# Performance work log

Hardware: AMD Instinct MI355X
Metric: run time of the kernel (lower is better)

The kernel has to match this reference:

```python
import math
import jax, jax.numpy as jnp
import numpy as np

B, T, C, H = 2, 2048, 1024, 16
D = C // H


def get_slopes(n):
    def pow2_slopes(n):
        start = 2.0 ** (-(2.0 ** (-(math.log2(n) - 3))))
        return [start * (start ** i) for i in range(n)]
    if math.log2(n).is_integer():
        return pow2_slopes(n)
    c = 2 ** math.floor(math.log2(n))
    return pow2_slopes(c) + get_slopes(2 * c)[0::2][: n - c]


def setup_inputs() -> dict:
    key = jax.random.key(0)
    ks = jax.random.split(key, 5)
    std = 0.02
    x = jax.random.normal(ks[0], (B, T, C), dtype=jnp.float32)
    Wq = std * jax.random.normal(ks[1], (C, C), dtype=jnp.float32)
    Wk = std * jax.random.normal(ks[2], (C, C), dtype=jnp.float32)
    Wv = std * jax.random.normal(ks[3], (C, C), dtype=jnp.float32)
    Wo = (std / math.sqrt(24)) * jax.random.normal(ks[4], (C, C), dtype=jnp.float32)
    z = jnp.zeros((C,), dtype=jnp.float32)
    return {"x": x, "Wq": Wq, "bq": z, "Wk": Wk, "bk": z, "Wv": Wv, "bv": z, "Wo": Wo, "bo": z}


def reference(x, Wq, bq, Wk, bk, Wv, bv, Wo, bo):
    b, t, c = x.shape
    h, d = H, c // H
    # qkv projections: nn.Linear computes x @ W.T + b
    q = (x @ Wq.T + bq).reshape(b, t, h, d).transpose(0, 2, 1, 3)  # [B,H,T,D]
    k = (x @ Wk.T + bk).reshape(b, t, h, d).transpose(0, 2, 1, 3)
    v = (x @ Wv.T + bv).reshape(b, t, h, d).transpose(0, 2, 1, 3)

    att = jnp.einsum("bhqd,bhkd->bhqk", q, k) * (1.0 / math.sqrt(d))

    # ALiBi bias: -slope_h * (i - j) on the lower triangle, 0 above
    slopes = jnp.asarray(get_slopes(h), dtype=x.dtype)  # [H]
    i = jnp.arange(t)
    rel = jnp.tril(i[:, None] - i[None, :]).astype(x.dtype)  # [T,T]
    alibi = -slopes[:, None, None] * rel  # [H,T,T]
    att = att + alibi[None, :, :, :]

    causal = jnp.tril(jnp.ones((t, t), dtype=bool))
    att = jnp.where(causal[None, None, :, :], att, -jnp.inf)
    att = jax.nn.softmax(att, axis=-1)

    y = jnp.einsum("bhqk,bhkd->bhqd", att, v)
    y = y.transpose(0, 2, 1, 3).reshape(b, t, c)
    return y @ Wo.T + bo
```

## Files before the change

### kernel.cpp

```cpp
#include <hip/hip_runtime.h>
#include <hip/hip_bf16.h>
#include <cstdint>
#include <cstddef>

#define B_ 2
#define T_ 2048
#define C_ 1024
#define H_ 16
#define D_ 64
#define BT_ (B_*T_)
#define QKV_S 3072

typedef __bf16 bf16;
typedef __bf16 bf16x4 __attribute__((ext_vector_type(4)));
typedef __bf16 bf16x8 __attribute__((ext_vector_type(8)));
typedef float f32x4 __attribute__((ext_vector_type(4)));

__global__ __launch_bounds__(256) void cast_all(const float* __restrict__ x,
                                                const float* __restrict__ wq,
                                                const float* __restrict__ wk,
                                                const float* __restrict__ wv,
                                                const float* __restrict__ wo,
                                                const float* __restrict__ bq,
                                                const float* __restrict__ bk,
                                                const float* __restrict__ bv,
                                                bf16* __restrict__ xb,
                                                bf16* __restrict__ wqkvb,
                                                bf16* __restrict__ wob,
                                                float* __restrict__ bqkv) {
  const int X4 = (BT_ * C_) / 4;
  const int W4 = (C_ * C_) / 4;
  int i = blockIdx.x * blockDim.x + threadIdx.x;
  if (i >= X4 + 4 * W4 + 768) return;
  if (i >= X4 + 4 * W4) {
    int idx = i - (X4 + 4 * W4);
    int w = idx >> 8, off = idx & 255;
    const float* src = (w == 0) ? bq : (w == 1) ? bk : bv;
    reinterpret_cast<float4*>(bqkv + w * C_)[off] = reinterpret_cast<const float4*>(src)[off];
    return;
  }
  const float* src;
  bf16* dst;
  int off;
  if (i < X4) {
    src = x; dst = xb; off = i;
  } else {
    int k = i - X4;
    int w = k >> 18;
    off = k & (W4 - 1);
    src = (w == 0) ? wq : (w == 1) ? wk : (w == 2) ? wv : wo;
    dst = (w < 3) ? (wqkvb + (size_t)w * C_ * C_) : wob;
  }
  float4 v = reinterpret_cast<const float4*>(src)[off];
  bf16x4 o;
  o[0] = (bf16)v.x; o[1] = (bf16)v.y; o[2] = (bf16)v.z; o[3] = (bf16)v.w;
  *reinterpret_cast<bf16x4*>(dst + (size_t)off * 4) = o;
}

template<typename OutT, bool FUSE_VT>
__global__ __launch_bounds__(256) void gemm_bt(const bf16* __restrict__ A,
                                               const bf16* __restrict__ Bm,
                                               const float* __restrict__ bias,
                                               OutT* __restrict__ Cout,
                                               bf16* __restrict__ VtOut,
                                               int M, int N, int K) {
  __shared__ bf16 As[3][128 * 32];
  __shared__ bf16 Bs[3][128 * 32];
  const int tid = threadIdx.x;
  const int wid = tid >> 6, lane = tid & 63;
  const int grp = lane >> 4, li = lane & 15;
  const int wr = wid >> 1, wc = wid & 1;
  const int m0 = blockIdx.y * 128, n0 = blockIdx.x * 128;

  f32x4 acc[4][4] = {};

  const int srow = lane >> 2;
  const int scol = (lane & 3) * 8;

  auto stage = [&](int k0, int bufi) __attribute__((always_inline)) {
#pragma unroll
    for (int p = 0; p < 2; ++p) {
      const int rbase = (p * 4 + wid) * 16;
      const bf16* ga = A + (size_t)(m0 + rbase + srow) * K + (k0 + scol);
      const bf16* gb = Bm + (size_t)(n0 + rbase + srow) * K + (k0 + scol);
      __builtin_amdgcn_global_load_lds((__attribute__((address_space(1))) void*)ga,
                                       (__attribute__((address_space(3))) void*)(&As[bufi][(p * 4 + wid) * 512]), 16, 0, 0);
      __builtin_amdgcn_global_load_lds((__attribute__((address_space(1))) void*)gb,
                                       (__attribute__((address_space(3))) void*)(&Bs[bufi][(p * 4 + wid) * 512]), 16, 0, 0);
    }
  };

  const int nt = K >> 5;
  stage(0, 0);
  if (nt > 1) stage(32, 1);
  int r = 0;
  for (int t = 0; t < nt; ++t) {
    if (t + 1 < nt) asm volatile("s_waitcnt vmcnt(4)\ns_barrier" ::: "memory");
    else            asm volatile("s_waitcnt vmcnt(0)\ns_barrier" ::: "memory");
    if (t + 2 < nt) stage((t + 2) * 32, (r == 0) ? 2 : r - 1);

    bf16x8 af[4], bfr[4];
#pragma unroll
    for (int m = 0; m < 4; ++m)
      af[m] = *reinterpret_cast<const bf16x8*>(&As[r][(wr * 64 + m * 16 + li) * 32 + grp * 8]);
#pragma unroll
    for (int n = 0; n < 4; ++n)
      bfr[n] = *reinterpret_cast<const bf16x8*>(&Bs[r][(wc * 64 + n * 16 + li) * 32 + grp * 8]);
#pragma unroll
    for (int m = 0; m < 4; ++m)
#pragma unroll
      for (int n = 0; n < 4; ++n)
        acc[m][n] = __builtin_amdgcn_mfma_f32_16x16x32_bf16(af[m], bfr[n], acc[m][n], 0, 0, 0);

    r = (r == 2) ? 0 : r + 1;
  }

  float bcol[4];
#pragma unroll
  for (int n = 0; n < 4; ++n) bcol[n] = bias[n0 + wc * 64 + n * 16 + li];

  if (FUSE_VT && n0 >= 2 * C_) {
#pragma unroll
    for (int m = 0; m < 4; ++m) {
      const int row0 = m0 + wr * 64 + m * 16 + grp * 4;
      const int b = row0 >> 11, t = row0 & (T_ - 1);
#pragma unroll
      for (int n = 0; n < 4; ++n) {
        const int hd = (n0 - 2 * C_) + wc * 64 + n * 16 + li;
        bf16x4 o4;
#pragma unroll
        for (int j = 0; j < 4; ++j) o4[j] = (bf16)(acc[m][n][j] + bcol[n]);
        *reinterpret_cast<bf16x4*>(VtOut + ((size_t)(b * C_ + hd)) * T_ + t) = o4;
      }
    }
  } else {
#pragma unroll
    for (int m = 0; m < 4; ++m) {
#pragma unroll
      for (int n = 0; n < 4; ++n) {
        const int col = n0 + wc * 64 + n * 16 + li;
#pragma unroll
        for (int j = 0; j < 4; ++j) {
          const int row = m0 + wr * 64 + m * 16 + grp * 4 + j;
          float v = acc[m][n][j] + bcol[n];
          Cout[(size_t)row * N + col] = (OutT)v;
        }
      }
    }
  }
}

__global__ __launch_bounds__(512) void attn_kernel(const bf16* __restrict__ qkv,
                                                   const bf16* __restrict__ Vt,
                                                   bf16* __restrict__ Y) {
  __shared__ bf16 Ks[3][64 * 64];
  __shared__ bf16 Vs[3][64 * 64];
  __shared__ bf16 Ps[8 * 16 * 72];

  const int tid = threadIdx.x;
  const int wid = tid >> 6, lane = tid & 63;
  const int grp = lane >> 4, li = lane & 15;
  const int QT = gridDim.x - 1 - blockIdx.x;
  const int bh = blockIdx.y;
  const int b = bh >> 4, h = bh & 15;
  const int q0 = QT * 128;
  const int wq0 = q0 + wid * 16;
  const int qi = wq0 + li;
  const float slope = exp2f(-0.5f * (float)(h + 1));

  bf16* Pw = Ps + wid * (16 * 72);

  bf16x8 qf[2];
  {
    const bf16* qrow = qkv + (size_t)(b * T_ + qi) * QKV_S + h * D_;
    qf[0] = *reinterpret_cast<const bf16x8*>(qrow + grp * 8);
    qf[1] = *reinterpret_cast<const bf16x8*>(qrow + 32 + grp * 8);
#pragma unroll
    for (int c = 0; c < 2; ++c)
#pragma unroll
      for (int j = 0; j < 8; ++j)
        qf[c][j] = (bf16)((float)qf[c][j] * 0.125f);
  }

  f32x4 oacc[4] = {};
  float mrun = -1e30f, lrun = 0.f;

  const bf16* Kbase = qkv + (size_t)b * T_ * QKV_S + C_ + (size_t)h * D_;
  const bf16* Vbase = Vt + (size_t)bh * D_ * T_;

  const int strow = tid >> 3;
  const int stswz = ((tid & 7) * 16) ^ ((strow & 7) << 4);
  const int rsw = (li & 7) << 4;

  auto stage = [&](int kv0, int bufi) __attribute__((always_inline)) {
    const bf16* gk = Kbase + (size_t)(kv0 + strow) * QKV_S + (stswz >> 1);
    const bf16* gv = Vbase + (size_t)strow * T_ + kv0 + (stswz >> 1);
    __builtin_amdgcn_global_load_lds((__attribute__((address_space(1))) void*)gk,
                                     (__attribute__((address_space(3))) void*)(&Ks[bufi][wid * 512]), 16, 0, 0);
    __builtin_amdgcn_global_load_lds((__attribute__((address_space(1))) void*)gv,
                                     (__attribute__((address_space(3))) void*)(&Vs[bufi][wid * 512]), 16, 0, 0);
  };

  auto compute = [&](int kv0, int bufi, bool masked) __attribute__((always_inline)) {
    const char* Kb = (const char*)&Ks[bufi][0];
    const char* Vb = (const char*)&Vs[bufi][0];

    f32x4 s[4] = {};
    __builtin_amdgcn_s_setprio(1);
#pragma unroll
    for (int n = 0; n < 4; ++n) {
      const char* kr = Kb + (n * 16 + li) * 128;
      bf16x8 kf0 = *reinterpret_cast<const bf16x8*>(kr + ((grp * 16) ^ rsw));
      bf16x8 kf1 = *reinterpret_cast<const bf16x8*>(kr + ((64 + grp * 16) ^ rsw));
      s[n] = __builtin_amdgcn_mfma_f32_16x16x32_bf16(kf0, qf[0], s[n], 0, 0, 0);
      s[n] = __builtin_amdgcn_mfma_f32_16x16x32_bf16(kf1, qf[1], s[n], 0, 0, 0);
    }
    __builtin_amdgcn_s_setprio(0);

    float p[4][4];
    float rm = -1e30f;
#pragma unroll
    for (int n = 0; n < 4; ++n)
#pragma unroll
      for (int j = 0; j < 4; ++j) {
        const int kv = kv0 + n * 16 + grp * 4 + j;
        float sv = fmaf(-slope, (float)(qi - kv), s[n][j]);
        if (masked) sv = (kv <= qi) ? sv : -1e30f;
        p[n][j] = sv;
        rm = fmaxf(rm, sv);
      }
    rm = fmaxf(rm, __shfl_xor(rm, 16, 64));
    rm = fmaxf(rm, __shfl_xor(rm, 32, 64));
    if (!__all(rm - mrun <= 8.0f)) {
      const float mnew = fmaxf(mrun, rm);
      const float alpha = __expf(mrun - mnew);
      mrun = mnew;
      lrun *= alpha;
#pragma unroll
      for (int nd = 0; nd < 4; ++nd)
#pragma unroll
        for (int j = 0; j < 4; ++j)
          oacc[nd][j] *= alpha;
    }
    float rs = 0.f;
#pragma unroll
    for (int n = 0; n < 4; ++n)
#pragma unroll
      for (int j = 0; j < 4; ++j) {
        float e = __expf(p[n][j] - mrun);
        p[n][j] = e;
        rs += e;
      }
    rs += __shfl_xor(rs, 16, 64);
    rs += __shfl_xor(rs, 32, 64);
    lrun += rs;

#pragma unroll
    for (int n = 0; n < 4; ++n) {
      bf16x4 p4;
#pragma unroll
      for (int j = 0; j < 4; ++j) p4[j] = (bf16)p[n][j];
      *reinterpret_cast<bf16x4*>(Pw + li * 72 + n * 16 + grp * 4) = p4;
    }
    asm volatile("s_waitcnt lgkmcnt(0)" ::: "memory");
    __builtin_amdgcn_sched_barrier(0);

    __builtin_amdgcn_s_setprio(1);
#pragma unroll
    for (int kc = 0; kc < 2; ++kc) {
      bf16x8 pb = *reinterpret_cast<const bf16x8*>(Pw + li * 72 + kc * 32 + grp * 8);
#pragma unroll
      for (int nd = 0; nd < 4; ++nd) {
        const char* vrp = Vb + (nd * 16 + li) * 128;
        bf16x8 vf = *reinterpret_cast<const bf16x8*>(vrp + ((kc * 64 + grp * 16) ^ rsw));
        oacc[nd] = __builtin_amdgcn_mfma_f32_16x16x32_bf16(vf, pb, oacc[nd], 0, 0, 0);
      }
    }
    __builtin_amdgcn_s_setprio(0);
  };

  const int nt = 2 * QT + 2;
  stage((nt - 1) * 64, 0);
  stage((nt - 2) * 64, 1);
  int r = 0;
  for (int t = 0; t < nt; ++t) {
    if (t + 1 < nt) asm volatile("s_waitcnt vmcnt(2)\ns_barrier" ::: "memory");
    else            asm volatile("s_waitcnt vmcnt(0)\ns_barrier" ::: "memory");
    if (t + 2 < nt) stage((nt - 3 - t) * 64, (r == 0) ? 2 : r - 1);
    const int kv0 = (nt - 1 - t) * 64;
    if (kv0 <= wq0) compute(kv0, r, kv0 + 64 > wq0);
    r = (r == 2) ? 0 : r + 1;
  }

  const float rinv = 1.f / lrun;
#pragma unroll
  for (int nd = 0; nd < 4; ++nd) {
    bf16x4 o4;
#pragma unroll
    for (int j = 0; j < 4; ++j) o4[j] = (bf16)(oacc[nd][j] * rinv);
    *reinterpret_cast<bf16x4*>(Pw + li * 72 + nd * 16 + grp * 4) = o4;
  }
  asm volatile("s_waitcnt lgkmcnt(0)" ::: "memory");
  __builtin_amdgcn_sched_barrier(0);
  {
    bf16* yrow = Y + (size_t)(b * T_ + qi) * C_ + h * D_;
#pragma unroll
    for (int c = 0; c < 2; ++c) {
      bf16x8 y8 = *reinterpret_cast<const bf16x8*>(Pw + li * 72 + (c * 4 + grp) * 8);
      *reinterpret_cast<bf16x8*>(yrow + (c * 4 + grp) * 8) = y8;
    }
  }
}

extern "C" void kernel_launch(void* const* d_in, const int* in_sizes, int n_in,
                              void* d_out, int out_size, void* d_ws, size_t ws_size,
                              hipStream_t stream) {
  const float* x  = (const float*)d_in[0];
  const float* Wq = (const float*)d_in[1];
  const float* bq = (const float*)d_in[2];
  const float* Wk = (const float*)d_in[3];
  const float* bk = (const float*)d_in[4];
  const float* Wv = (const float*)d_in[5];
  const float* bv = (const float*)d_in[6];
  const float* Wo = (const float*)d_in[7];
  const float* bo = (const float*)d_in[8];
  float* out = (float*)d_out;

  char* ws = (char*)d_ws;
  bf16* xb    = (bf16*)ws; ws += (size_t)BT_ * C_ * 2;
  bf16* wqkvb = (bf16*)ws; ws += (size_t)3 * C_ * C_ * 2;
  bf16* wob   = (bf16*)ws; ws += (size_t)C_ * C_ * 2;
  bf16* qkvb  = (bf16*)ws; ws += (size_t)BT_ * QKV_S * 2;
  bf16* vtb   = (bf16*)ws; ws += (size_t)B_ * H_ * D_ * T_ * 2;
  float* bqkv = (float*)ws; ws += (size_t)3 * C_ * 4;
  bf16* yb    = xb;

  {
    const int total = (BT_ * C_ + 4 * C_ * C_) / 4 + 768;
    cast_all<<<dim3((total + 255) / 256), dim3(256), 0, stream>>>(
        x, Wq, Wk, Wv, Wo, bq, bk, bv, xb, wqkvb, wob, bqkv);
  }

  gemm_bt<bf16, true><<<dim3(QKV_S / 128, BT_ / 128), dim3(256), 0, stream>>>(
      xb, wqkvb, bqkv, qkvb, vtb, BT_, QKV_S, C_);

  attn_kernel<<<dim3(T_ / 128, B_ * H_), dim3(512), 0, stream>>>(qkvb, vtb, yb);

  gemm_bt<float, false><<<dim3(C_ / 128, BT_ / 128), dim3(256), 0, stream>>>(
      yb, wob, bo, out, nullptr, BT_, C_, C_);
}
```

Baseline: 226.1 us.

## Add dedicated QKV GEMM with 128x256 tiles and swizzled direct-to-LDS loads

After: 266.3 us. 1.18x slower.

```diff
diff --git a/kernel.cpp b/kernel.cpp
--- a/kernel.cpp
+++ b/kernel.cpp
@@ -58,11 +58,109 @@
 }
 
 template<typename OutT, bool FUSE_VT>
+__global__ __launch_bounds__(256) void gemm_qkv(const bf16* __restrict__ A,
+                                                const bf16* __restrict__ Bm,
+                                                const float* __restrict__ bias,
+                                                OutT* __restrict__ Cout,
+                                                bf16* __restrict__ VtOut,
+                                                int M, int N, int K) {
+  __shared__ bf16 As[3][128 * 32];
+  __shared__ bf16 Bs[3][256 * 32];
+  const int tid = threadIdx.x;
+  const int wid = tid >> 6, lane = tid & 63;
+  const int grp = lane >> 4, li = lane & 15;
+  const int wr = wid >> 1, wc = wid & 1;
+  const int m0 = blockIdx.y * 128, n0 = blockIdx.x * 256;
+
+  f32x4 acc[4][8] = {};
+
+  const int rl = lane >> 2;
+  const int soff = ((((lane & 3) * 16) ^ ((rl & 3) << 4)) >> 1);
+
+  auto stage = [&](int k0, int bufi) __attribute__((always_inline)) {
+#pragma unroll
+    for (int p = 0; p < 2; ++p) {
+      const bf16* ga = A + (size_t)(m0 + p * 64 + wid * 16 + rl) * K + k0 + soff;
+      __builtin_amdgcn_global_load_lds((__attribute__((address_space(1))) void*)ga,
+                                       (__attribute__((address_space(3))) void*)(&As[bufi][p * 2048 + wid * 512]), 16, 0, 0);
+    }
+#pragma unroll
+    for (int p = 0; p < 4; ++p) {
+      const bf16* gb = Bm + (size_t)(n0 + p * 64 + wid * 16 + rl) * K + k0 + soff;
+      __builtin_amdgcn_global_load_lds((__attribute__((address_space(1))) void*)gb,
+                                       (__attribute__((address_space(3))) void*)(&Bs[bufi][p * 2048 + wid * 512]), 16, 0, 0);
+    }
+  };
+
+  const int rdx = ((grp * 8) ^ ((li & 3) << 3));
+
+  const int nt = K >> 5;
+  stage(0, 0);
+  stage(32, 1);
+  int r = 0;
+  for (int t = 0; t < nt; ++t) {
+    if (t + 1 < nt) asm volatile("s_waitcnt vmcnt(6)\ns_barrier" ::: "memory");
+    else            asm volatile("s_waitcnt vmcnt(0)\ns_barrier" ::: "memory");
+    if (t + 2 < nt) stage((t + 2) * 32, (r == 0) ? 2 : r - 1);
+
+    bf16x8 af[4], bfr[8];
+#pragma unroll
+    for (int m = 0; m < 4; ++m)
+      af[m] = *reinterpret_cast<const bf16x8*>(&As[r][(wr * 64 + m * 16 + li) * 32 + rdx]);
+#pragma unroll
+    for (int n = 0; n < 8; ++n)
+      bfr[n] = *reinterpret_cast<const bf16x8*>(&Bs[r][(wc * 128 + n * 16 + li) * 32 + rdx]);
+    __builtin_amdgcn_s_setprio(1);
+#pragma unroll
+    for (int m = 0; m < 4; ++m)
+#pragma unroll
+      for (int n = 0; n < 8; ++n)
+        acc[m][n] = __builtin_amdgcn_mfma_f32_16x16x32_bf16(af[m], bfr[n], acc[m][n], 0, 0, 0);
+    __builtin_amdgcn_s_setprio(0);
+
+    r = (r == 2) ? 0 : r + 1;
+  }
+
+  float bcol[8];
+#pragma unroll
+  for (int n = 0; n < 8; ++n) bcol[n] = bias[n0 + wc * 128 + n * 16 + li];
+
+  if (FUSE_VT && n0 >= 2 * C_) {
+#pragma unroll
+    for (int m = 0; m < 4; ++m) {
+      const int row0 = m0 + wr * 64 + m * 16 + grp * 4;
+      const int b = row0 >> 11, t = row0 & (T_ - 1);
+#pragma unroll
+      for (int n = 0; n < 8; ++n) {
+        const int hd = (n0 - 2 * C_) + wc * 128 + n * 16 + li;
+        bf16x4 o4;
+#pragma unroll
+        for (int j = 0; j < 4; ++j) o4[j] = (bf16)(acc[m][n][j] + bcol[n]);
+        *reinterpret_cast<bf16x4*>(VtOut + ((size_t)(b * C_ + hd)) * T_ + t) = o4;
+      }
+    }
+  } else {
+#pragma unroll
+    for (int m = 0; m < 4; ++m) {
+#pragma unroll
+      for (int n = 0; n < 8; ++n) {
+        const int col = n0 + wc * 128 + n * 16 + li;
+#pragma unroll
+        for (int j = 0; j < 4; ++j) {
+          const int row = m0 + wr * 64 + m * 16 + grp * 4 + j;
+          float v = acc[m][n][j] + bcol[n];
+          Cout[(size_t)row * N + col] = (OutT)v;
+        }
+      }
+    }
+  }
+}
+
+template<typename OutT>
 __global__ __launch_bounds__(256) void gemm_bt(const bf16* __restrict__ A,
                                                const bf16* __restrict__ Bm,
                                                const float* __restrict__ bias,
                                                OutT* __restrict__ Cout,
-                                               bf16* __restrict__ VtOut,
                                                int M, int N, int K) {
   __shared__ bf16 As[3][128 * 32];
   __shared__ bf16 Bs[3][128 * 32];
@@ -118,33 +216,16 @@
   float bcol[4];
 #pragma unroll
   for (int n = 0; n < 4; ++n) bcol[n] = bias[n0 + wc * 64 + n * 16 + li];
-
-  if (FUSE_VT && n0 >= 2 * C_) {
-#pragma unroll
-    for (int m = 0; m < 4; ++m) {
-      const int row0 = m0 + wr * 64 + m * 16 + grp * 4;
-      const int b = row0 >> 11, t = row0 & (T_ - 1);
-#pragma unroll
-      for (int n = 0; n < 4; ++n) {
-        const int hd = (n0 - 2 * C_) + wc * 64 + n * 16 + li;
-        bf16x4 o4;
-#pragma unroll
-        for (int j = 0; j < 4; ++j) o4[j] = (bf16)(acc[m][n][j] + bcol[n]);
-        *reinterpret_cast<bf16x4*>(VtOut + ((size_t)(b * C_ + hd)) * T_ + t) = o4;
-      }
-    }
-  } else {
-#pragma unroll
-    for (int m = 0; m < 4; ++m) {
-#pragma unroll
-      for (int n = 0; n < 4; ++n) {
-        const int col = n0 + wc * 64 + n * 16 + li;
-#pragma unroll
-        for (int j = 0; j < 4; ++j) {
-          const int row = m0 + wr * 64 + m * 16 + grp * 4 + j;
-          float v = acc[m][n][j] + bcol[n];
-          Cout[(size_t)row * N + col] = (OutT)v;
-        }
+#pragma unroll
+  for (int m = 0; m < 4; ++m) {
+#pragma unroll
+    for (int n = 0; n < 4; ++n) {
+      const int col = n0 + wc * 64 + n * 16 + li;
+#pragma unroll
+      for (int j = 0; j < 4; ++j) {
+        const int row = m0 + wr * 64 + m * 16 + grp * 4 + j;
+        float v = acc[m][n][j] + bcol[n];
+        Cout[(size_t)row * N + col] = (OutT)v;
       }
     }
   }
@@ -341,11 +422,11 @@
         x, Wq, Wk, Wv, Wo, bq, bk, bv, xb, wqkvb, wob, bqkv);
   }
 
-  gemm_bt<bf16, true><<<dim3(QKV_S / 128, BT_ / 128), dim3(256), 0, stream>>>(
+  gemm_qkv<bf16, true><<<dim3(QKV_S / 256, BT_ / 128), dim3(256), 0, stream>>>(
       xb, wqkvb, bqkv, qkvb, vtb, BT_, QKV_S, C_);
 
   attn_kernel<<<dim3(T_ / 128, B_ * H_), dim3(512), 0, stream>>>(qkvb, vtb, yb);
 
-  gemm_bt<float, false><<<dim3(C_ / 128, BT_ / 128), dim3(256), 0, stream>>>(
-      yb, wob, bo, out, nullptr, BT_, C_, C_);
+  gemm_bt<float><<<dim3(C_ / 128, BT_ / 128), dim3(256), 0, stream>>>(
+      yb, wob, bo, out, BT_, C_, C_);
 }
```
